# Performance work log

Measured on AMD Instinct MI355X. Metric: run time of the kernel, lower is better.

Reference implementation:

```python
import jax, jax.numpy as jnp
import numpy as np

NUM_HEADS = 8
NUM_POINTS = 4


def _grid_sample_bilinear(img, grid, H, W):
    """torch F.grid_sample(mode='bilinear', padding='zeros', align_corners=False).
    img:  [B, H, W, D]   grid: [B, S, 2] with (x, y) in [-1, 1].
    Returns [B, S, D].
    """
    gx, gy = grid[..., 0], grid[..., 1]
    # align_corners=False pixel mapping
    x = ((gx + 1.0) * W - 1.0) * 0.5
    y = ((gy + 1.0) * H - 1.0) * 0.5
    x0 = jnp.floor(x)
    y0 = jnp.floor(y)
    wx1 = x - x0
    wy1 = y - y0
    x0i = x0.astype(jnp.int32)
    y0i = y0.astype(jnp.int32)
    img_flat = img.reshape(img.shape[0], H * W, img.shape[-1])  # [B, N, D]

    def corner(xi, yi, w):
        valid = (xi >= 0) & (xi < W) & (yi >= 0) & (yi < H)  # zeros padding
        idx = jnp.clip(yi, 0, H - 1) * W + jnp.clip(xi, 0, W - 1)  # [B, S]
        v = jnp.take_along_axis(img_flat, idx[..., None], axis=1)  # [B, S, D]
        return v * (w * valid.astype(img.dtype))[..., None]

    out = corner(x0i, y0i, (1.0 - wx1) * (1.0 - wy1))
    out += corner(x0i + 1, y0i, wx1 * (1.0 - wy1))
    out += corner(x0i, y0i + 1, (1.0 - wx1) * wy1)
    out += corner(x0i + 1, y0i + 1, wx1 * wy1)
    return out


def setup_inputs() -> dict:
    key = jax.random.key(0)
    ks = jax.random.split(key, 12)
    B, Q, D = 4, 1024, 256
    H, W = 128, 128
    nh, npts = NUM_HEADS, NUM_POINTS
    f32 = jnp.float32
    return {
        "query": jax.random.normal(ks[0], (B, Q, D), f32),
        "reference_points": jax.random.uniform(ks[1], (B, Q, 2), f32),
        "value": jax.random.normal(ks[2], (B, H * W, D), f32),
        "W_off": jax.random.normal(ks[3], (D, nh * npts * 2), f32) * 0.02,
        "b_off": jax.random.normal(ks[4], (nh * npts * 2,), f32) * 0.02,
        "W_attn": jax.random.normal(ks[5], (D, nh * npts), f32) * 0.02,
        "b_attn": jax.random.normal(ks[6], (nh * npts,), f32) * 0.02,
        "W_v": jax.random.normal(ks[7], (D, D), f32) * (D ** -0.5),
        "b_v": jnp.zeros((D,), f32),
        "W_out": jax.random.normal(ks[8], (nh * D, D), f32) * ((nh * D) ** -0.5),
        "b_out": jnp.zeros((D,), f32),
        "H": H,
        "W": W,
    }


def reference(query, reference_points, value, W_off, b_off, W_attn, b_attn,
              W_v, b_v, W_out, b_out, H, W):
    B, Q, D = query.shape
    nh, npts = NUM_HEADS, NUM_POINTS
    # learned offsets and per-point attention weights
    offsets = (query @ W_off + b_off).reshape(B, Q, nh, npts, 2)
    attn = jax.nn.softmax((query @ W_attn + b_attn).reshape(B, Q, nh, npts), axis=-1)
    # sampling locations in [-1, 1]
    locs = reference_points[:, :, None, None, :] + offsets * 0.1
    locs = jnp.clip(locs, 0.0, 1.0) * 2.0 - 1.0
    # value projection -> 2D feature map [B, H, W, D]
    img = (value @ W_v + b_v).reshape(B, H, W, D)
    # sample all heads/points at once
    grid = locs.reshape(B, Q * nh * npts, 2)
    sampled = _grid_sample_bilinear(img, grid, H, W).reshape(B, Q, nh, npts, D)
    # weighted reduce over points, concat heads
    weighted = jnp.einsum("bqhpd,bqhp->bqhd", sampled, attn)
    out = weighted.reshape(B, Q, nh * D) @ W_out + b_out
    return out
```

## Files before the change

### kernel.cpp

```cpp
#include <hip/hip_runtime.h>
#include <hip/hip_bf16.h>
#include <math.h>

constexpr int B  = 4;
constexpr int Q  = 1024;
constexpr int D  = 256;
constexpr int NH = 8;
constexpr int NP = 4;
constexpr int H  = 128;
constexpr int W  = 128;
constexpr int HW = H * W;
constexpr int KAUG = 2112;

typedef short   bf16x8  __attribute__((ext_vector_type(8)));
typedef float   f32x4   __attribute__((ext_vector_type(4)));
typedef short   short4v __attribute__((ext_vector_type(4)));
typedef unsigned short ushort8v __attribute__((ext_vector_type(8)));

__device__ inline unsigned short f2bf(float f) {
    union { float f; unsigned u; } v; v.f = f;
    unsigned r = v.u + 0x7fff + ((v.u >> 16) & 1);
    return (unsigned short)(r >> 16);
}
__device__ inline float bf2f(unsigned short s) {
    union { unsigned u; float f; } v; v.u = ((unsigned)s) << 16;
    return v.f;
}

__device__ inline void async16(const void* g, void* l) {
    __builtin_amdgcn_global_load_lds(
        (const __attribute__((address_space(1))) unsigned*)g,
        (__attribute__((address_space(3))) unsigned*)l, 16, 0, 0);
}

constexpr int RB_CONV  = 0;
constexpr int RB_WOA   = RB_CONV  + (B * HW * D) / 1024;
constexpr int RB_BIAS  = RB_WOA   + (D * 128) / 256;
constexpr int RB_CONVT = RB_BIAS  + 1;
constexpr int RB_WV    = RB_CONVT + (NH * D * D) / 256;
constexpr int RB_BV    = RB_WV    + (D * D) / 1024;
constexpr int RB_END   = RB_BV    + (D * 64) / 256;

__global__ __launch_bounds__(256)
void k_prep(const float* __restrict__ value,
            const float* __restrict__ W_off,  const float* __restrict__ b_off,
            const float* __restrict__ W_attn, const float* __restrict__ b_attn,
            const float* __restrict__ b_v,    const float* __restrict__ W_out,
            const float* __restrict__ W_v,
            unsigned short* __restrict__ val_bf,
            float* __restrict__ Woa,
            float* __restrict__ bias_oa,
            unsigned short* __restrict__ Wout_t,
            unsigned short* __restrict__ Wv_bf,
            unsigned short* __restrict__ WcT) {
    const int blk = blockIdx.x;
    const int tid = threadIdx.x;

    if (blk < RB_WOA) {
        const int i = (blk * 1024) + tid * 4;
        const float4 v = *(const float4*)&value[i];
        short4v o;
        o.x = (short)f2bf(v.x); o.y = (short)f2bf(v.y);
        o.z = (short)f2bf(v.z); o.w = (short)f2bf(v.w);
        *(short4v*)&val_bf[i] = o;
    } else if (blk < RB_BIAS) {
        const int i = (blk - RB_WOA) * 256 + tid;
        const int k = i >> 7, j = i & 127;
        float v = 0.0f;
        if (j < 64)      v = W_off[k * 64 + j];
        else if (j < 96) v = W_attn[k * 32 + (j - 64)];
        Woa[i] = v;
    } else if (blk < RB_CONVT) {
        if (tid < 128) {
            float v = 0.0f;
            if (tid < 64)      v = b_off[tid];
            else if (tid < 96) v = b_attn[tid - 64];
            bias_oa[tid] = v;
        }
    } else if (blk < RB_WV) {
        const int i = (blk - RB_CONVT) * 256 + tid;
        const int n = i >> 11, k = i & 2047;
        Wout_t[i] = f2bf(W_out[(size_t)k * D + n]);
    } else if (blk < RB_BV) {
        const int i = (blk - RB_WV) * 1024 + tid * 4;
        const float4 v = *(const float4*)&W_v[i];
        short4v o;
        o.x = (short)f2bf(v.x); o.y = (short)f2bf(v.y);
        o.z = (short)f2bf(v.z); o.w = (short)f2bf(v.w);
        *(short4v*)&Wv_bf[i] = o;
    } else {
        const int t = (blk - RB_BV) * 256 + tid;
        const int n = t >> 6, c = t & 63;
        float v = 0.0f;
        if (c < 8) {
            #pragma unroll 8
            for (int j = 0; j < D; ++j)
                v += b_v[j] * W_out[((size_t)c * D + j) * D + n];
        }
        WcT[(size_t)n * KAUG + 2048 + c] = f2bf(v);
    }
}

#define BM 64
#define BN 64
#define BK 16

__global__ __launch_bounds__(256)
void k_sgemm(const float* __restrict__ A, const float* __restrict__ Bm,
             const float* __restrict__ bias, float* __restrict__ C,
             int M, int N, int K) {
    __shared__ __align__(16) float As[BK][BM + 4];
    __shared__ __align__(16) float Bs[BK][BN + 4];

    const int t  = threadIdx.x;
    const int tx = t & 15;
    const int ty = t >> 4;
    const int m0 = blockIdx.x * BM;
    const int n0 = blockIdx.y * BN;

    const int arow = t >> 2;
    const int akg  = (t & 3) * 4;
    const int brow = t >> 4;
    const int bcol = (t & 15) * 4;

    float acc[4][4] = {};

    for (int k0 = 0; k0 < K; k0 += BK) {
        const float4 av = *(const float4*)&A[(size_t)(m0 + arow) * K + k0 + akg];
        const float4 bv = *(const float4*)&Bm[(size_t)(k0 + brow) * N + n0 + bcol];
        __syncthreads();
        As[akg + 0][arow] = av.x;
        As[akg + 1][arow] = av.y;
        As[akg + 2][arow] = av.z;
        As[akg + 3][arow] = av.w;
        *(float4*)&Bs[brow][bcol] = bv;
        __syncthreads();

        #pragma unroll
        for (int kk = 0; kk < BK; ++kk) {
            const float4 a = *(const float4*)&As[kk][ty * 4];
            const float4 b = *(const float4*)&Bs[kk][tx * 4];
            acc[0][0] += a.x * b.x; acc[0][1] += a.x * b.y; acc[0][2] += a.x * b.z; acc[0][3] += a.x * b.w;
            acc[1][0] += a.y * b.x; acc[1][1] += a.y * b.y; acc[1][2] += a.y * b.z; acc[1][3] += a.y * b.w;
            acc[2][0] += a.z * b.x; acc[2][1] += a.z * b.y; acc[2][2] += a.z * b.z; acc[2][3] += a.z * b.w;
            acc[3][0] += a.w * b.x; acc[3][1] += a.w * b.y; acc[3][2] += a.w * b.z; acc[3][3] += a.w * b.w;
        }
    }

    const float4 bb = *(const float4*)&bias[n0 + tx * 4];
    #pragma unroll
    for (int i = 0; i < 4; ++i) {
        const int m = m0 + ty * 4 + i;
        float4 r;
        r.x = acc[i][0] + bb.x;
        r.y = acc[i][1] + bb.y;
        r.z = acc[i][2] + bb.z;
        r.w = acc[i][3] + bb.w;
        *(float4*)&C[(size_t)m * N + n0 + tx * 4] = r;
    }
}

template <int OUTMODE>
__global__ __launch_bounds__(256)
void k_gemm64(const unsigned short* __restrict__ A, int lda,
              const unsigned short* __restrict__ Bt, int ldb,
              const float* __restrict__ bias,
              void* __restrict__ Cout, int ldc, int K) {
    __shared__ __align__(16) unsigned short lds[4][4096];

    const int tid  = threadIdx.x;
    const int lane = tid & 63;
    const int w    = tid >> 6;
    const int wm   = w >> 1, wn = w & 1;
    const int m0 = blockIdx.x * 64, n0 = blockIdx.y * 64;
    if (OUTMODE == 1) Bt += (size_t)blockIdx.z * 256;

    const int srow = w * 8 + (lane >> 3);
    const int schk = (lane & 7) ^ (lane >> 3);
    const unsigned short* ag0 = A  + (size_t)(m0 + srow)      * lda + schk * 8;
    const unsigned short* ag1 = A  + (size_t)(m0 + srow + 32) * lda + schk * 8;
    const unsigned short* bg0 = Bt + (size_t)(n0 + srow)      * ldb + schk * 8;
    const unsigned short* bg1 = Bt + (size_t)(n0 + srow + 32) * ldb + schk * 8;
    const int l0 = w * 512 + lane * 8;
    const int l1 = l0 + 2048;

    int aoff[2][2], boff[2][2];
    #pragma unroll
    for (int i = 0; i < 2; ++i)
        #pragma unroll
        for (int kk = 0; kk < 2; ++kk) {
            const int ar = wm * 32 + i * 16 + (lane & 15);
            aoff[i][kk] = ar * 64 + ((((lane >> 4) + kk * 4) ^ (ar & 7)) * 8);
            const int br = wn * 32 + i * 16 + (lane & 15);
            boff[i][kk] = br * 64 + ((((lane >> 4) + kk * 4) ^ (br & 7)) * 8);
        }

    f32x4 acc[2][2];
    #pragma unroll
    for (int i = 0; i < 2; ++i)
        #pragma unroll
        for (int j = 0; j < 2; ++j) acc[i][j] = (f32x4){0.f, 0.f, 0.f, 0.f};

    async16(ag0, &lds[0][l0]); async16(ag1, &lds[0][l1]);
    async16(bg0, &lds[1][l0]); async16(bg1, &lds[1][l1]);

    const int niter = K >> 6;
    for (int it = 0; it < niter; ++it) {
        __syncthreads();
        const int cur = (it & 1) * 2;
        if (it + 1 < niter) {
            const int nxt = 2 - cur;
            const int ko  = (it + 1) * 64;
            async16(ag0 + ko, &lds[nxt][l0]);
            async16(ag1 + ko, &lds[nxt][l1]);
            async16(bg0 + ko, &lds[nxt + 1][l0]);
            async16(bg1 + ko, &lds[nxt + 1][l1]);
        }
        bf16x8 af[2][2], bfv[2][2];
        #pragma unroll
        for (int i = 0; i < 2; ++i)
            #pragma unroll
            for (int kk = 0; kk < 2; ++kk) {
                af[i][kk]  = *(const bf16x8*)&lds[cur][aoff[i][kk]];
                bfv[i][kk] = *(const bf16x8*)&lds[cur + 1][boff[i][kk]];
            }
        #pragma unroll
        for (int i = 0; i < 2; ++i)
            #pragma unroll
            for (int j = 0; j < 2; ++j)
                #pragma unroll
                for (int kk = 0; kk < 2; ++kk)
                    acc[i][j] = __builtin_amdgcn_mfma_f32_16x16x32_bf16(
                        af[i][kk], bfv[j][kk], acc[i][j], 0, 0, 0);
    }

    const int colb = n0 + wn * 32 + (lane & 15);
    const int rowb = m0 + wm * 32 + (lane >> 4) * 4;
    if (OUTMODE == 0) {
        float* C = (float*)Cout;
        #pragma unroll
        for (int j = 0; j < 2; ++j) {
            const int col = colb + j * 16;
            const float bb = bias[col];
            #pragma unroll
            for (int i = 0; i < 2; ++i)
                #pragma unroll
                for (int r = 0; r < 4; ++r)
                    C[(size_t)(rowb + i * 16 + r) * ldc + col] = acc[i][j][r] + bb;
        }
    } else {
        unsigned short* Wt = (unsigned short*)Cout;
        const int ocol = blockIdx.z * 256;
        #pragma unroll
        for (int j = 0; j < 2; ++j) {
            const int col = colb + j * 16;
            #pragma unroll
            for (int i = 0; i < 2; ++i)
                #pragma unroll
                for (int r = 0; r < 4; ++r)
                    Wt[(size_t)col * ldc + ocol + rowb + i * 16 + r] =
                        f2bf(acc[i][j][r]);
        }
    }
}

__global__ __launch_bounds__(256)
void k_sample(const unsigned short* __restrict__ val,
              const float* __restrict__ raw,
              const float* __restrict__ refpts,
              unsigned short* __restrict__ sv) {
    const int bq   = blockIdx.x;
    const int b    = bq >> 10;
    const int tid  = threadIdx.x;
    const int lane = tid & 63;
    const int w    = tid >> 6;

    __shared__ float s_raw[128];
    __shared__ int   s_off[128];
    __shared__ float s_wgt[128];

    if (tid < 128) s_raw[tid] = raw[(size_t)bq * 128 + tid];
    __syncthreads();

    if (tid < NH * NP) {
        const int h = tid >> 2;
        float m = -1e30f;
        #pragma unroll
        for (int p = 0; p < NP; ++p) m = fmaxf(m, s_raw[64 + h * 4 + p]);
        float s = 0.0f;
        #pragma unroll
        for (int p = 0; p < NP; ++p) s += __expf(s_raw[64 + h * 4 + p] - m);
        const float a = __expf(s_raw[64 + tid] - m) / s;

        const float refx = refpts[(size_t)bq * 2 + 0];
        const float refy = refpts[(size_t)bq * 2 + 1];
        const float gx = fminf(fmaxf(refx + s_raw[tid * 2 + 0] * 0.1f, 0.0f), 1.0f) * 2.0f - 1.0f;
        const float gy = fminf(fmaxf(refy + s_raw[tid * 2 + 1] * 0.1f, 0.0f), 1.0f) * 2.0f - 1.0f;
        const float x  = ((gx + 1.0f) * (float)W - 1.0f) * 0.5f;
        const float y  = ((gy + 1.0f) * (float)H - 1.0f) * 0.5f;
        const float x0f = floorf(x), y0f = floorf(y);
        const float wx1 = x - x0f,  wy1 = y - y0f;
        const float wx0 = 1.0f - wx1, wy0 = 1.0f - wy1;
        const int x0 = (int)x0f, y0 = (int)y0f;
        const int x1 = x0 + 1,  y1 = y0 + 1;
        const float vx0 = (x0 >= 0 && x0 < W) ? 1.0f : 0.0f;
        const float vx1 = (x1 >= 0 && x1 < W) ? 1.0f : 0.0f;
        const float vy0 = (y0 >= 0 && y0 < H) ? 1.0f : 0.0f;
        const float vy1 = (y1 >= 0 && y1 < H) ? 1.0f : 0.0f;
        const int xc0 = min(max(x0, 0), W - 1);
        const int xc1 = min(max(x1, 0), W - 1);
        const int yc0 = min(max(y0, 0), H - 1);
        const int yc1 = min(max(y1, 0), H - 1);
        s_off[tid * 4 + 0] = yc0 * W + xc0;
        s_off[tid * 4 + 1] = yc0 * W + xc1;
        s_off[tid * 4 + 2] = yc1 * W + xc0;
        s_off[tid * 4 + 3] = yc1 * W + xc1;
        s_wgt[tid * 4 + 0] = a * wx0 * wy0 * vx0 * vy0;
        s_wgt[tid * 4 + 1] = a * wx1 * wy0 * vx1 * vy0;
        s_wgt[tid * 4 + 2] = a * wx0 * wy1 * vx0 * vy1;
        s_wgt[tid * 4 + 3] = a * wx1 * wy1 * vx1 * vy1;
    }
    __syncthreads();

    if (tid < 8) {
        float S = 0.0f;
        #pragma unroll
        for (int c = 0; c < 16; ++c) S += s_wgt[tid * 16 + c];
        sv[(size_t)bq * KAUG + 2048 + tid] = f2bf(S);
    } else if (tid < 64) {
        sv[(size_t)bq * KAUG + 2048 + tid] = 0;
    }

    const int half = lane >> 5;
    const int l5   = lane & 31;
    const unsigned short* ib = val + (size_t)b * HW * D + l5 * 8;

    float acc[2][8] = {};
    #pragma unroll
    for (int g = 0; g < 2; ++g) {
        ushort8v vb[8];
        float    wg[8];
        #pragma unroll
        for (int j = 0; j < 8; ++j) {
            const int flat = w * 32 + (g * 8 + j) * 2 + half;
            wg[j] = s_wgt[flat];
            vb[j] = *(const ushort8v*)(ib + (size_t)s_off[flat] * D);
        }
        #pragma unroll
        for (int j = 0; j < 8; ++j)
            #pragma unroll
            for (int k = 0; k < 8; ++k)
                acc[g][k] += wg[j] * bf2f(vb[j][k]);
    }

    #pragma unroll
    for (int hh = 0; hh < 2; ++hh) {
        float comb[8];
        #pragma unroll
        for (int k = 0; k < 8; ++k)
            comb[k] = acc[hh][k] + __shfl_xor(acc[hh][k], 32, 64);
        if (half == 0) {
            const int h = w * 2 + hh;
            ushort8v o;
            #pragma unroll
            for (int k = 0; k < 8; ++k) o[k] = f2bf(comb[k]);
            *(ushort8v*)&sv[(size_t)bq * KAUG + h * D + l5 * 8] = o;
        }
    }
}

extern "C" void kernel_launch(void* const* d_in, const int* in_sizes, int n_in,
                              void* d_out, int out_size, void* d_ws, size_t ws_size,
                              hipStream_t stream) {
    const float* query  = (const float*)d_in[0];
    const float* refpts = (const float*)d_in[1];
    const float* value  = (const float*)d_in[2];
    const float* W_off  = (const float*)d_in[3];
    const float* b_off  = (const float*)d_in[4];
    const float* W_attn = (const float*)d_in[5];
    const float* b_attn = (const float*)d_in[6];
    const float* W_v    = (const float*)d_in[7];
    const float* b_v    = (const float*)d_in[8];
    const float* W_out  = (const float*)d_in[9];
    const float* b_out  = (const float*)d_in[10];
    float* out = (float*)d_out;

    char* wsb = (char*)d_ws;
    unsigned short* val_bf  = (unsigned short*)(wsb);
    unsigned short* sv      = (unsigned short*)(wsb + 33554432);
    unsigned short* WcT     = (unsigned short*)(wsb + 50855936);
    unsigned short* Wout_t  = (unsigned short*)(wsb + 51937280);
    unsigned short* Wv_bf   = (unsigned short*)(wsb + 52985856);
    float*          raw     = (float*)(wsb + 53116928);
    float*          Woa     = (float*)(wsb + 55214080);
    float*          bias_oa = (float*)(wsb + 55345152);

    k_prep<<<RB_END, 256, 0, stream>>>(value, W_off, b_off, W_attn, b_attn,
                                       b_v, W_out, W_v,
                                       val_bf, Woa, bias_oa, Wout_t, Wv_bf, WcT);

    {
        dim3 grid((B * Q) / BM, 128 / BN);
        k_sgemm<<<grid, 256, 0, stream>>>(query, Woa, bias_oa, raw,
                                          B * Q, 128, D);
    }

    {
        dim3 grid(D / 64, D / 64, NH);
        k_gemm64<1><<<grid, 256, 0, stream>>>(Wv_bf, D, Wout_t, NH * D,
                                              nullptr, WcT, KAUG, D);
    }

    k_sample<<<B * Q, 256, 0, stream>>>(val_bf, raw, refpts, sv);

    {
        dim3 grid((B * Q) / 64, D / 64, 1);
        k_gemm64<0><<<grid, 256, 0, stream>>>(sv, KAUG, WcT, KAUG,
                                              b_out, out, D, KAUG);
    }
}
```

Baseline: 197.2 us.

## Merge five launches into three by co-scheduling independent stages in shared grids

The prep conversion kernel and the offset/attention SGEMM are merged into one launch, with the SGEMM reading W_off/W_attn and the biases directly instead of a padded staging copy. The weight-combining GEMM (W_v x W_out) is folded into the sampling kernel as extra blocks. The GEMM body becomes a device function so it can run inside both launches. This cuts launch count and inter-kernel serialization gaps but puts heterogeneous block types in one grid, which can create load imbalance and raise per-block LDS allocation for the sampling blocks.

```diff
diff --git a/kernel.cpp b/kernel.cpp
--- a/kernel.cpp
+++ b/kernel.cpp
@@ -33,147 +33,19 @@
         (__attribute__((address_space(3))) unsigned*)l, 16, 0, 0);
 }
 
-constexpr int RB_CONV  = 0;
-constexpr int RB_WOA   = RB_CONV  + (B * HW * D) / 1024;
-constexpr int RB_BIAS  = RB_WOA   + (D * 128) / 256;
-constexpr int RB_CONVT = RB_BIAS  + 1;
-constexpr int RB_WV    = RB_CONVT + (NH * D * D) / 256;
-constexpr int RB_BV    = RB_WV    + (D * D) / 1024;
-constexpr int RB_END   = RB_BV    + (D * 64) / 256;
-
-__global__ __launch_bounds__(256)
-void k_prep(const float* __restrict__ value,
-            const float* __restrict__ W_off,  const float* __restrict__ b_off,
-            const float* __restrict__ W_attn, const float* __restrict__ b_attn,
-            const float* __restrict__ b_v,    const float* __restrict__ W_out,
-            const float* __restrict__ W_v,
-            unsigned short* __restrict__ val_bf,
-            float* __restrict__ Woa,
-            float* __restrict__ bias_oa,
-            unsigned short* __restrict__ Wout_t,
-            unsigned short* __restrict__ Wv_bf,
-            unsigned short* __restrict__ WcT) {
-    const int blk = blockIdx.x;
-    const int tid = threadIdx.x;
-
-    if (blk < RB_WOA) {
-        const int i = (blk * 1024) + tid * 4;
-        const float4 v = *(const float4*)&value[i];
-        short4v o;
-        o.x = (short)f2bf(v.x); o.y = (short)f2bf(v.y);
-        o.z = (short)f2bf(v.z); o.w = (short)f2bf(v.w);
-        *(short4v*)&val_bf[i] = o;
-    } else if (blk < RB_BIAS) {
-        const int i = (blk - RB_WOA) * 256 + tid;
-        const int k = i >> 7, j = i & 127;
-        float v = 0.0f;
-        if (j < 64)      v = W_off[k * 64 + j];
-        else if (j < 96) v = W_attn[k * 32 + (j - 64)];
-        Woa[i] = v;
-    } else if (blk < RB_CONVT) {
-        if (tid < 128) {
-            float v = 0.0f;
-            if (tid < 64)      v = b_off[tid];
-            else if (tid < 96) v = b_attn[tid - 64];
-            bias_oa[tid] = v;
-        }
-    } else if (blk < RB_WV) {
-        const int i = (blk - RB_CONVT) * 256 + tid;
-        const int n = i >> 11, k = i & 2047;
-        Wout_t[i] = f2bf(W_out[(size_t)k * D + n]);
-    } else if (blk < RB_BV) {
-        const int i = (blk - RB_WV) * 1024 + tid * 4;
-        const float4 v = *(const float4*)&W_v[i];
-        short4v o;
-        o.x = (short)f2bf(v.x); o.y = (short)f2bf(v.y);
-        o.z = (short)f2bf(v.z); o.w = (short)f2bf(v.w);
-        *(short4v*)&Wv_bf[i] = o;
-    } else {
-        const int t = (blk - RB_BV) * 256 + tid;
-        const int n = t >> 6, c = t & 63;
-        float v = 0.0f;
-        if (c < 8) {
-            #pragma unroll 8
-            for (int j = 0; j < D; ++j)
-                v += b_v[j] * W_out[((size_t)c * D + j) * D + n];
-        }
-        WcT[(size_t)n * KAUG + 2048 + c] = f2bf(v);
-    }
-}
-
-#define BM 64
-#define BN 64
-#define BK 16
-
-__global__ __launch_bounds__(256)
-void k_sgemm(const float* __restrict__ A, const float* __restrict__ Bm,
-             const float* __restrict__ bias, float* __restrict__ C,
-             int M, int N, int K) {
-    __shared__ __align__(16) float As[BK][BM + 4];
-    __shared__ __align__(16) float Bs[BK][BN + 4];
-
-    const int t  = threadIdx.x;
-    const int tx = t & 15;
-    const int ty = t >> 4;
-    const int m0 = blockIdx.x * BM;
-    const int n0 = blockIdx.y * BN;
-
-    const int arow = t >> 2;
-    const int akg  = (t & 3) * 4;
-    const int brow = t >> 4;
-    const int bcol = (t & 15) * 4;
-
-    float acc[4][4] = {};
-
-    for (int k0 = 0; k0 < K; k0 += BK) {
-        const float4 av = *(const float4*)&A[(size_t)(m0 + arow) * K + k0 + akg];
-        const float4 bv = *(const float4*)&Bm[(size_t)(k0 + brow) * N + n0 + bcol];
-        __syncthreads();
-        As[akg + 0][arow] = av.x;
-        As[akg + 1][arow] = av.y;
-        As[akg + 2][arow] = av.z;
-        As[akg + 3][arow] = av.w;
-        *(float4*)&Bs[brow][bcol] = bv;
-        __syncthreads();
-
-        #pragma unroll
-        for (int kk = 0; kk < BK; ++kk) {
-            const float4 a = *(const float4*)&As[kk][ty * 4];
-            const float4 b = *(const float4*)&Bs[kk][tx * 4];
-            acc[0][0] += a.x * b.x; acc[0][1] += a.x * b.y; acc[0][2] += a.x * b.z; acc[0][3] += a.x * b.w;
-            acc[1][0] += a.y * b.x; acc[1][1] += a.y * b.y; acc[1][2] += a.y * b.z; acc[1][3] += a.y * b.w;
-            acc[2][0] += a.z * b.x; acc[2][1] += a.z * b.y; acc[2][2] += a.z * b.z; acc[2][3] += a.z * b.w;
-            acc[3][0] += a.w * b.x; acc[3][1] += a.w * b.y; acc[3][2] += a.w * b.z; acc[3][3] += a.w * b.w;
-        }
-    }
-
-    const float4 bb = *(const float4*)&bias[n0 + tx * 4];
-    #pragma unroll
-    for (int i = 0; i < 4; ++i) {
-        const int m = m0 + ty * 4 + i;
-        float4 r;
-        r.x = acc[i][0] + bb.x;
-        r.y = acc[i][1] + bb.y;
-        r.z = acc[i][2] + bb.z;
-        r.w = acc[i][3] + bb.w;
-        *(float4*)&C[(size_t)m * N + n0 + tx * 4] = r;
-    }
-}
-
 template <int OUTMODE>
-__global__ __launch_bounds__(256)
-void k_gemm64(const unsigned short* __restrict__ A, int lda,
-              const unsigned short* __restrict__ Bt, int ldb,
-              const float* __restrict__ bias,
-              void* __restrict__ Cout, int ldc, int K) {
-    __shared__ __align__(16) unsigned short lds[4][4096];
-
+__device__ __forceinline__ void gemm64_body(
+        unsigned short* __restrict__ lds,
+        const unsigned short* __restrict__ A, int lda,
+        const unsigned short* __restrict__ Bt, int ldb,
+        const float* __restrict__ bias,
+        void* __restrict__ Cout, int ldc, int K,
+        int m0, int n0, int zblk) {
     const int tid  = threadIdx.x;
     const int lane = tid & 63;
     const int w    = tid >> 6;
     const int wm   = w >> 1, wn = w & 1;
-    const int m0 = blockIdx.x * 64, n0 = blockIdx.y * 64;
-    if (OUTMODE == 1) Bt += (size_t)blockIdx.z * 256;
+    if (OUTMODE == 1) Bt += (size_t)zblk * 256;
 
     const int srow = w * 8 + (lane >> 3);
     const int schk = (lane & 7) ^ (lane >> 3);
@@ -201,8 +73,8 @@
         #pragma unroll
         for (int j = 0; j < 2; ++j) acc[i][j] = (f32x4){0.f, 0.f, 0.f, 0.f};
 
-    async16(ag0, &lds[0][l0]); async16(ag1, &lds[0][l1]);
-    async16(bg0, &lds[1][l0]); async16(bg1, &lds[1][l1]);
+    async16(ag0, &lds[0 * 4096 + l0]); async16(ag1, &lds[0 * 4096 + l1]);
+    async16(bg0, &lds[1 * 4096 + l0]); async16(bg1, &lds[1 * 4096 + l1]);
 
     const int niter = K >> 6;
     for (int it = 0; it < niter; ++it) {
@@ -211,18 +83,18 @@
         if (it + 1 < niter) {
             const int nxt = 2 - cur;
             const int ko  = (it + 1) * 64;
-            async16(ag0 + ko, &lds[nxt][l0]);
-            async16(ag1 + ko, &lds[nxt][l1]);
-            async16(bg0 + ko, &lds[nxt + 1][l0]);
-            async16(bg1 + ko, &lds[nxt + 1][l1]);
+            async16(ag0 + ko, &lds[nxt * 4096 + l0]);
+            async16(ag1 + ko, &lds[nxt * 4096 + l1]);
+            async16(bg0 + ko, &lds[(nxt + 1) * 4096 + l0]);
+            async16(bg1 + ko, &lds[(nxt + 1) * 4096 + l1]);
         }
         bf16x8 af[2][2], bfv[2][2];
         #pragma unroll
         for (int i = 0; i < 2; ++i)
             #pragma unroll
             for (int kk = 0; kk < 2; ++kk) {
-                af[i][kk]  = *(const bf16x8*)&lds[cur][aoff[i][kk]];
-                bfv[i][kk] = *(const bf16x8*)&lds[cur + 1][boff[i][kk]];
+                af[i][kk]  = *(const bf16x8*)&lds[cur * 4096 + aoff[i][kk]];
+                bfv[i][kk] = *(const bf16x8*)&lds[(cur + 1) * 4096 + boff[i][kk]];
             }
         #pragma unroll
         for (int i = 0; i < 2; ++i)
@@ -250,7 +122,7 @@
         }
     } else {
         unsigned short* Wt = (unsigned short*)Cout;
-        const int ocol = blockIdx.z * 256;
+        const int ocol = zblk * 256;
         #pragma unroll
         for (int j = 0; j < 2; ++j) {
             const int col = colb + j * 16;
@@ -264,20 +136,146 @@
     }
 }
 
+constexpr int R1_CONV = 0;
+constexpr int R1_SG   = R1_CONV + (B * HW * D) / 1024;
+constexpr int R1_WOUT = R1_SG   + 128;
+constexpr int R1_WV   = R1_WOUT + (NH * D * D) / 256;
+constexpr int R1_BV   = R1_WV   + (D * D) / 1024;
+constexpr int R1_END  = R1_BV   + (D * 64) / 256;
+
 __global__ __launch_bounds__(256)
-void k_sample(const unsigned short* __restrict__ val,
+void k_stage1(const float* __restrict__ value,
+              const float* __restrict__ query,
+              const float* __restrict__ W_off,  const float* __restrict__ b_off,
+              const float* __restrict__ W_attn, const float* __restrict__ b_attn,
+              const float* __restrict__ b_v,    const float* __restrict__ W_out,
+              const float* __restrict__ W_v,
+              unsigned short* __restrict__ val_bf,
+              float* __restrict__ raw,
+              unsigned short* __restrict__ Wout_t,
+              unsigned short* __restrict__ Wv_bf,
+              unsigned short* __restrict__ WcT) {
+    __shared__ __align__(16) float smem[2][16][68];
+    const int blk = blockIdx.x;
+    const int tid = threadIdx.x;
+
+    if (blk < R1_SG) {
+        const int i = (blk * 1024) + tid * 4;
+        const float4 v = *(const float4*)&value[i];
+        short4v o;
+        o.x = (short)f2bf(v.x); o.y = (short)f2bf(v.y);
+        o.z = (short)f2bf(v.z); o.w = (short)f2bf(v.w);
+        *(short4v*)&val_bf[i] = o;
+    } else if (blk < R1_WOUT) {
+        const int blkr = blk - R1_SG;
+        const int m0 = (blkr >> 1) * 64;
+        const int n0 = (blkr & 1) * 64;
+        float (*As)[68] = smem[0];
+        float (*Bs)[68] = smem[1];
+        const int t  = tid;
+        const int tx = t & 15, ty = t >> 4;
+        const int arow = t >> 2, akg = (t & 3) * 4;
+        const int brow = t >> 4, bcol = (t & 15) * 4;
+
+        float acc[4][4] = {};
+        for (int k0 = 0; k0 < D; k0 += 16) {
+            const float4 av = *(const float4*)&query[(size_t)(m0 + arow) * D + k0 + akg];
+            const int kr = k0 + brow;
+            const int j  = n0 + bcol;
+            float4 bv;
+            if (j < 64)      bv = *(const float4*)&W_off[kr * 64 + j];
+            else if (j < 96) bv = *(const float4*)&W_attn[kr * 32 + (j - 64)];
+            else             bv = (float4){0.f, 0.f, 0.f, 0.f};
+            __syncthreads();
+            As[akg + 0][arow] = av.x;
+            As[akg + 1][arow] = av.y;
+            As[akg + 2][arow] = av.z;
+            As[akg + 3][arow] = av.w;
+            *(float4*)&Bs[brow][bcol] = bv;
+            __syncthreads();
+            #pragma unroll
+            for (int kk = 0; kk < 16; ++kk) {
+                const float4 a = *(const float4*)&As[kk][ty * 4];
+                const float4 b = *(const float4*)&Bs[kk][tx * 4];
+                acc[0][0] += a.x * b.x; acc[0][1] += a.x * b.y; acc[0][2] += a.x * b.z; acc[0][3] += a.x * b.w;
+                acc[1][0] += a.y * b.x; acc[1][1] += a.y * b.y; acc[1][2] += a.y * b.z; acc[1][3] += a.y * b.w;
+                acc[2][0] += a.z * b.x; acc[2][1] += a.z * b.y; acc[2][2] += a.z * b.z; acc[2][3] += a.z * b.w;
+                acc[3][0] += a.w * b.x; acc[3][1] += a.w * b.y; acc[3][2] += a.w * b.z; acc[3][3] += a.w * b.w;
+            }
+        }
+        float bb[4];
+        #pragma unroll
+        for (int c = 0; c < 4; ++c) {
+            const int col = n0 + tx * 4 + c;
+            bb[c] = (col < 64) ? b_off[col] : ((col < 96) ? b_attn[col - 64] : 0.0f);
+        }
+        #pragma unroll
+        for (int i = 0; i < 4; ++i) {
+            const int m = m0 + ty * 4 + i;
+            float4 r;
+            r.x = acc[i][0] + bb[0];
+            r.y = acc[i][1] + bb[1];
+            r.z = acc[i][2] + bb[2];
+            r.w = acc[i][3] + bb[3];
+            *(float4*)&raw[(size_t)m * 128 + n0 + tx * 4] = r;
+        }
+    } else if (blk < R1_WV) {
+        const int i = (blk - R1_WOUT) * 256 + tid;
+        const int n = i >> 11, k = i & 2047;
+        Wout_t[i] = f2bf(W_out[(size_t)k * D + n]);
+    } else if (blk < R1_BV) {
+        const int i = (blk - R1_WV) * 1024 + tid * 4;
+        const float4 v = *(const float4*)&W_v[i];
+        short4v o;
+        o.x = (short)f2bf(v.x); o.y = (short)f2bf(v.y);
+        o.z = (short)f2bf(v.z); o.w = (short)f2bf(v.w);
+        *(short4v*)&Wv_bf[i] = o;
+    } else {
+        const int t = (blk - R1_BV) * 256 + tid;
+        const int n = t >> 6, c = t & 63;
+        float v = 0.0f;
+        if (c < 8) {
+            #pragma unroll 8
+            for (int j = 0; j < D; ++j)
+                v += b_v[j] * W_out[((size_t)c * D + j) * D + n];
+        }
+        WcT[(size_t)n * KAUG + 2048 + c] = f2bf(v);
+    }
+}
+
+constexpr int R2_WC  = B * Q;
+constexpr int R2_END = R2_WC + 128;
+
+__global__ __launch_bounds__(256)
+void k_stage2(const unsigned short* __restrict__ val,
               const float* __restrict__ raw,
               const float* __restrict__ refpts,
-              unsigned short* __restrict__ sv) {
-    const int bq   = blockIdx.x;
+              const unsigned short* __restrict__ Wv_bf,
+              const unsigned short* __restrict__ Wout_t,
+              unsigned short* __restrict__ sv,
+              unsigned short* __restrict__ WcT) {
+    __shared__ __align__(16) unsigned short smem[16384];
+    const int blk = blockIdx.x;
+    const int tid = threadIdx.x;
+
+    if (blk >= R2_WC) {
+        const int blkr = blk - R2_WC;
+        const int z  = blkr >> 4;
+        const int m0 = ((blkr >> 2) & 3) * 64;
+        const int n0 = (blkr & 3) * 64;
+        gemm64_body<1>(smem, Wv_bf, D, Wout_t, NH * D, nullptr, WcT, KAUG, D,
+                       m0, n0, z);
+        return;
+    }
+
+    const int bq   = blk;
     const int b    = bq >> 10;
-    const int tid  = threadIdx.x;
     const int lane = tid & 63;
     const int w    = tid >> 6;
 
-    __shared__ float s_raw[128];
-    __shared__ int   s_off[128];
-    __shared__ float s_wgt[128];
+    float* s_raw = (float*)smem;
+    int*   s_off = (int*)((char*)smem + 512);
+    float* s_wgt = (float*)((char*)smem + 1024);
 
     if (tid < 128) s_raw[tid] = raw[(size_t)bq * 128 + tid];
     __syncthreads();
@@ -369,6 +367,16 @@
     }
 }
 
+__global__ __launch_bounds__(256)
+void k_stage3(const unsigned short* __restrict__ sv,
+              const unsigned short* __restrict__ WcT,
+              const float* __restrict__ b_out,
+              float* __restrict__ out) {
+    __shared__ __align__(16) unsigned short smem[16384];
+    gemm64_body<0>(smem, sv, KAUG, WcT, KAUG, b_out, out, D, KAUG,
+                   blockIdx.x * 64, blockIdx.y * 64, 0);
+}
+
 extern "C" void kernel_launch(void* const* d_in, const int* in_sizes, int n_in,
                               void* d_out, int out_size, void* d_ws, size_t ws_size,
                               hipStream_t stream) {
@@ -392,30 +400,16 @@
     unsigned short* Wout_t  = (unsigned short*)(wsb + 51937280);
     unsigned short* Wv_bf   = (unsigned short*)(wsb + 52985856);
     float*          raw     = (float*)(wsb + 53116928);
-    float*          Woa     = (float*)(wsb + 55214080);
-    float*          bias_oa = (float*)(wsb + 55345152);
-
-    k_prep<<<RB_END, 256, 0, stream>>>(value, W_off, b_off, W_attn, b_attn,
-                                       b_v, W_out, W_v,
-                                       val_bf, Woa, bias_oa, Wout_t, Wv_bf, WcT);
+
+    k_stage1<<<R1_END, 256, 0, stream>>>(value, query, W_off, b_off,
+                                         W_attn, b_attn, b_v, W_out, W_v,
+                                         val_bf, raw, Wout_t, Wv_bf, WcT);
+
+    k_stage2<<<R2_END, 256, 0, stream>>>(val_bf, raw, refpts, Wv_bf, Wout_t,
+                                         sv, WcT);
 
     {
-        dim3 grid((B * Q) / BM, 128 / BN);
-        k_sgemm<<<grid, 256, 0, stream>>>(query, Woa, bias_oa, raw,
-                                          B * Q, 128, D);
-    }
-
-    {
-        dim3 grid(D / 64, D / 64, NH);
-        k_gemm64<1><<<grid, 256, 0, stream>>>(Wv_bf, D, Wout_t, NH * D,
-                                              nullptr, WcT, KAUG, D);
-    }
-
-    k_sample<<<B * Q, 256, 0, stream>>>(val_bf, raw, refpts, sv);
-
-    {
-        dim3 grid((B * Q) / 64, D / 64, 1);
-        k_gemm64<0><<<grid, 256, 0, stream>>>(sv, KAUG, WcT, KAUG,
-                                              b_out, out, D, KAUG);
-    }
-}
+        dim3 grid((B * Q) / 64, D / 64);
+        k_stage3<<<grid, 256, 0, stream>>>(sv, WcT, b_out, out);
+    }
+}
```

New measurement: 186.6 us. -5.4%, faster.
